# Kernel optimization log

Hardware: AMD Instinct MI355X
Metric: run time of the kernel (lower is better)

## Reference

```python
import jax, jax.numpy as jnp
import numpy as np

N_NODES = 100000
N_EDGES = 640000
IN_DIM = 128
HIDDEN = 256
OUT_DIM = 64


def setup_inputs() -> dict:
    key = jax.random.key(0)
    k_x, k_e, k_w1, k_b1, k_w2, k_b2 = jax.random.split(key, 6)
    x = jax.random.normal(k_x, (N_NODES, IN_DIM), dtype=jnp.float32)
    edge_index = jax.random.randint(k_e, (2, N_EDGES), 0, N_NODES, dtype=jnp.int32)
    # torch Linear init ~ U(-1/sqrt(fan_in), 1/sqrt(fan_in)); scale here is arbitrary for a correctness baseline
    s1 = 1.0 / np.sqrt(2 * IN_DIM)
    s2 = 1.0 / np.sqrt(HIDDEN)
    W1 = jax.random.uniform(k_w1, (2 * IN_DIM, HIDDEN), minval=-s1, maxval=s1, dtype=jnp.float32)
    b1 = jax.random.uniform(k_b1, (HIDDEN,), minval=-s1, maxval=s1, dtype=jnp.float32)
    W2 = jax.random.uniform(k_w2, (HIDDEN, OUT_DIM), minval=-s2, maxval=s2, dtype=jnp.float32)
    b2 = jax.random.uniform(k_b2, (OUT_DIM,), minval=-s2, maxval=s2, dtype=jnp.float32)
    return {"x": x, "edge_index": edge_index, "W1": W1, "b1": b1, "W2": W2, "b2": b2}


def reference(x, edge_index, W1, b1, W2, b2):
    # gather source/destination node features: [E, in_dim] each
    src = x[edge_index[0]]
    dst = x[edge_index[1]]
    h = jnp.concatenate([src, dst], axis=-1)      # [E, 2*in_dim]
    h = jax.nn.relu(h @ W1 + b1)                  # [E, hidden]
    return h @ W2 + b2                            # [E, out_dim]
```

## Files before the change

### kernel.cpp

```cpp
#include <hip/hip_runtime.h>
#include <hip/hip_bf16.h>


#define N_EDGES_C 640000
#define N_NODES_C 100000
#define IN_DIM_C  128
#define CAT_DIM_C 256
#define HIDDEN_C  256
#define OUT_DIM_C 64
#define BM        64
#define LDA       264

typedef __attribute__((ext_vector_type(8))) short bf16x8;
typedef __attribute__((ext_vector_type(4))) float f32x4;

__device__ __forceinline__ ushort f2bs(float f) {
  union { __hip_bfloat16 h; ushort u; } c;
  c.h = __float2bfloat16(f);
  return c.u;
}

__global__ __launch_bounds__(256) void cast_x_kernel(const float* __restrict__ x,
                                                     ushort* __restrict__ xb) {
  const int i = blockIdx.x * 256 + threadIdx.x;
  const float4 v0 = reinterpret_cast<const float4*>(x)[2 * i];
  const float4 v1 = reinterpret_cast<const float4*>(x)[2 * i + 1];
  uint4 o;
  o.x = (unsigned)f2bs(v0.x) | ((unsigned)f2bs(v0.y) << 16);
  o.y = (unsigned)f2bs(v0.z) | ((unsigned)f2bs(v0.w) << 16);
  o.z = (unsigned)f2bs(v1.x) | ((unsigned)f2bs(v1.y) << 16);
  o.w = (unsigned)f2bs(v1.z) | ((unsigned)f2bs(v1.w) << 16);
  reinterpret_cast<uint4*>(xb)[i] = o;
}

__global__ __launch_bounds__(256) void prep_w_kernel(const float* __restrict__ W1,
                                                     const float* __restrict__ W2,
                                                     ushort* __restrict__ W1t,
                                                     ushort* __restrict__ W2t) {
  const int i = blockIdx.x * 256 + threadIdx.x;
  if (i < HIDDEN_C * CAT_DIM_C) {
    const int n = i >> 8, k = i & 255;
    W1t[i] = f2bs(W1[k * HIDDEN_C + n]);
  } else {
    const int j = i - HIDDEN_C * CAT_DIM_C;
    const int o = j >> 8, k = j & 255;
    W2t[j] = f2bs(W2[k * OUT_DIM_C + o]);
  }
}

template <int USE_XB>
__global__ __launch_bounds__(256) void edge_ffn_kernel(
    const ushort* __restrict__ xb, const float* __restrict__ xf,
    const int* __restrict__ ei,
    const ushort* __restrict__ W1t, const float* __restrict__ b1,
    const ushort* __restrict__ W2t, const float* __restrict__ b2,
    float* __restrict__ out) {
  __shared__ ushort A[BM * LDA];

  const int tid  = threadIdx.x;
  const int lane = tid & 63;
  const int w    = tid >> 6;
  const int e0   = blockIdx.x * BM;
  const int l15  = lane & 15;
  const int lg   = lane >> 4;

  {
    const int li  = tid & 15;
    const int hr0 = tid >> 4;
#pragma unroll
    for (int it = 0; it < 8; ++it) {
      const int hr    = hr0 + it * 16;
      const int edge  = hr >> 1;
      const int which = hr & 1;
      const int node  = ei[which * N_EDGES_C + e0 + edge];
      ushort* dst = &A[edge * LDA + which * IN_DIM_C + li * 8];
      if (USE_XB) {
        *reinterpret_cast<uint4*>(dst) =
            *reinterpret_cast<const uint4*>(xb + node * IN_DIM_C + li * 8);
      } else {
        const float4* row = reinterpret_cast<const float4*>(xf + node * IN_DIM_C);
        const float4 v0 = row[li * 2];
        const float4 v1 = row[li * 2 + 1];
        uint4 o;
        o.x = (unsigned)f2bs(v0.x) | ((unsigned)f2bs(v0.y) << 16);
        o.y = (unsigned)f2bs(v0.z) | ((unsigned)f2bs(v0.w) << 16);
        o.z = (unsigned)f2bs(v1.x) | ((unsigned)f2bs(v1.y) << 16);
        o.w = (unsigned)f2bs(v1.z) | ((unsigned)f2bs(v1.w) << 16);
        *reinterpret_cast<uint4*>(dst) = o;
      }
    }
  }
  __syncthreads();

  f32x4 acc[4][4];
#pragma unroll
  for (int m = 0; m < 4; ++m)
#pragma unroll
    for (int n = 0; n < 4; ++n) acc[m][n] = (f32x4){0.f, 0.f, 0.f, 0.f};

#pragma unroll
  for (int ks = 0; ks < 8; ++ks) {
    const int kb = ks * 32 + lg * 8;
    bf16x8 a[4], b[4];
#pragma unroll
    for (int m = 0; m < 4; ++m)
      a[m] = *reinterpret_cast<const bf16x8*>(&A[(m * 16 + l15) * LDA + kb]);
#pragma unroll
    for (int n = 0; n < 4; ++n) {
      const int col = w * 64 + n * 16 + l15;
      b[n] = *reinterpret_cast<const bf16x8*>(W1t + col * CAT_DIM_C + kb);
    }
#pragma unroll
    for (int m = 0; m < 4; ++m)
#pragma unroll
      for (int n = 0; n < 4; ++n)
        acc[m][n] = __builtin_amdgcn_mfma_f32_16x16x32_bf16(a[m], b[n], acc[m][n], 0, 0, 0);
  }

  float b1v[4];
#pragma unroll
  for (int n = 0; n < 4; ++n) b1v[n] = b1[w * 64 + n * 16 + l15];

  __syncthreads();
#pragma unroll
  for (int m = 0; m < 4; ++m)
#pragma unroll
    for (int n = 0; n < 4; ++n)
#pragma unroll
      for (int i = 0; i < 4; ++i) {
        float v = acc[m][n][i] + b1v[n];
        v = v > 0.f ? v : 0.f;
        const int row = m * 16 + lg * 4 + i;
        const int col = w * 64 + n * 16 + l15;
        A[row * LDA + col] = f2bs(v);
      }
  __syncthreads();

  f32x4 acc2[4];
#pragma unroll
  for (int n = 0; n < 4; ++n) acc2[n] = (f32x4){0.f, 0.f, 0.f, 0.f};

#pragma unroll
  for (int ks = 0; ks < 8; ++ks) {
    const int kb = ks * 32 + lg * 8;
    const bf16x8 a2 = *reinterpret_cast<const bf16x8*>(&A[(w * 16 + l15) * LDA + kb]);
#pragma unroll
    for (int n = 0; n < 4; ++n) {
      const bf16x8 bb =
          *reinterpret_cast<const bf16x8*>(W2t + (n * 16 + l15) * HIDDEN_C + kb);
      acc2[n] = __builtin_amdgcn_mfma_f32_16x16x32_bf16(a2, bb, acc2[n], 0, 0, 0);
    }
  }

  float b2v[4];
#pragma unroll
  for (int n = 0; n < 4; ++n) b2v[n] = b2[n * 16 + l15];
#pragma unroll
  for (int n = 0; n < 4; ++n)
#pragma unroll
    for (int i = 0; i < 4; ++i) {
      const int row = e0 + w * 16 + lg * 4 + i;
      out[row * OUT_DIM_C + n * 16 + l15] = acc2[n][i] + b2v[n];
    }
}

extern "C" void kernel_launch(void* const* d_in, const int* in_sizes, int n_in,
                              void* d_out, int out_size, void* d_ws, size_t ws_size,
                              hipStream_t stream) {
  const float* x  = (const float*)d_in[0];
  const int*   ei = (const int*)d_in[1];
  const float* W1 = (const float*)d_in[2];
  const float* b1 = (const float*)d_in[3];
  const float* W2 = (const float*)d_in[4];
  const float* b2 = (const float*)d_in[5];
  float* out = (float*)d_out;

  const size_t xb_elems  = (size_t)N_NODES_C * IN_DIM_C;
  const size_t w1t_elems = HIDDEN_C * CAT_DIM_C;
  const size_t w2t_elems = OUT_DIM_C * HIDDEN_C;
  const size_t need_full = (xb_elems + w1t_elems + w2t_elems) * sizeof(ushort);

  ushort* base = (ushort*)d_ws;
  if (ws_size >= need_full) {
    ushort* xbp = base;
    ushort* W1t = xbp + xb_elems;
    ushort* W2t = W1t + w1t_elems;
    cast_x_kernel<<<(N_NODES_C * IN_DIM_C) / (256 * 8), 256, 0, stream>>>(x, xbp);
    prep_w_kernel<<<(HIDDEN_C * CAT_DIM_C + OUT_DIM_C * HIDDEN_C) / 256, 256, 0, stream>>>(
        W1, W2, W1t, W2t);
    edge_ffn_kernel<1><<<N_EDGES_C / BM, 256, 0, stream>>>(xbp, x, ei, W1t, b1, W2t, b2, out);
  } else {
    ushort* W1t = base;
    ushort* W2t = W1t + w1t_elems;
    prep_w_kernel<<<(HIDDEN_C * CAT_DIM_C + OUT_DIM_C * HIDDEN_C) / 256, 256, 0, stream>>>(
        W1, W2, W1t, W2t);
    edge_ffn_kernel<0><<<N_EDGES_C / BM, 256, 0, stream>>>(nullptr, x, ei, W1t, b1, W2t, b2, out);
  }
}
```

Baseline: 534.4 us.

## Make edge FFN kernel persistent over tiles with register-prefetched gathers

Each block now processes five 64-edge tiles instead of one, with the grid shrunk to cover that. The next tile's node-feature gather is issued into registers while the current tile's GEMMs run, and edge indices are loaded two tiles ahead, to hide gather latency. Bias loads are hoisted out of the tile loop and launch bounds request four blocks per CU. The cost is higher register pressure from the prefetch buffers and fewer, longer-running blocks.

New measurement: 1.129 ms. 2.11x slower.

```diff
diff --git a/kernel.cpp b/kernel.cpp
--- a/kernel.cpp
+++ b/kernel.cpp
@@ -10,6 +10,8 @@
 #define OUT_DIM_C 64
 #define BM        64
 #define LDA       264
+#define TPB_TILES 5
+#define GRID_MAIN 2000
 
 typedef __attribute__((ext_vector_type(8))) short bf16x8;
 typedef __attribute__((ext_vector_type(4))) float f32x4;
@@ -49,7 +51,7 @@
 }
 
 template <int USE_XB>
-__global__ __launch_bounds__(256) void edge_ffn_kernel(
+__global__ __launch_bounds__(256, 4) void edge_ffn_kernel(
     const ushort* __restrict__ xb, const float* __restrict__ xf,
     const int* __restrict__ ei,
     const ushort* __restrict__ W1t, const float* __restrict__ b1,
@@ -60,108 +62,133 @@
   const int tid  = threadIdx.x;
   const int lane = tid & 63;
   const int w    = tid >> 6;
-  const int e0   = blockIdx.x * BM;
   const int l15  = lane & 15;
   const int lg   = lane >> 4;
-
-  {
-    const int li  = tid & 15;
-    const int hr0 = tid >> 4;
+  const int li   = tid & 15;
+  const int hr0  = tid >> 4;
+  const int tile0 = blockIdx.x * TPB_TILES;
+
+  float b1v[4], b2v[4];
+#pragma unroll
+  for (int n = 0; n < 4; ++n) {
+    b1v[n] = b1[w * 64 + n * 16 + l15];
+    b2v[n] = b2[n * 16 + l15];
+  }
+
+  int   nid[8];
+  uint4 rbuf[8];
+
+#define LOAD_NID(tt)                                                        \
+  {                                                                         \
+    const int e0n = (tt) * BM;                                              \
+    _Pragma("unroll") for (int it = 0; it < 8; ++it) {                      \
+      const int hr = hr0 + it * 16;                                         \
+      nid[it] = ei[(hr & 1) * N_EDGES_C + e0n + (hr >> 1)];                 \
+    }                                                                       \
+  }
+
+#define GATHER()                                                            \
+  {                                                                         \
+    _Pragma("unroll") for (int it = 0; it < 8; ++it) {                      \
+      if (USE_XB) {                                                         \
+        rbuf[it] = *reinterpret_cast<const uint4*>(                         \
+            xb + (size_t)nid[it] * IN_DIM_C + li * 8);                      \
+      } else {                                                              \
+        const float4* row =                                                 \
+            reinterpret_cast<const float4*>(xf + (size_t)nid[it] * IN_DIM_C);\
+        const float4 v0 = row[li * 2];                                      \
+        const float4 v1 = row[li * 2 + 1];                                  \
+        uint4 o;                                                            \
+        o.x = (unsigned)f2bs(v0.x) | ((unsigned)f2bs(v0.y) << 16);          \
+        o.y = (unsigned)f2bs(v0.z) | ((unsigned)f2bs(v0.w) << 16);          \
+        o.z = (unsigned)f2bs(v1.x) | ((unsigned)f2bs(v1.y) << 16);          \
+        o.w = (unsigned)f2bs(v1.z) | ((unsigned)f2bs(v1.w) << 16);          \
+        rbuf[it] = o;                                                       \
+      }                                                                     \
+    }                                                                       \
+  }
+
+  LOAD_NID(tile0);
+  GATHER();
+  LOAD_NID(tile0 + 1);
+
+  for (int t = 0; t < TPB_TILES; ++t) {
+    const int e0 = (tile0 + t) * BM;
+
+    __syncthreads();
 #pragma unroll
     for (int it = 0; it < 8; ++it) {
-      const int hr    = hr0 + it * 16;
-      const int edge  = hr >> 1;
-      const int which = hr & 1;
-      const int node  = ei[which * N_EDGES_C + e0 + edge];
-      ushort* dst = &A[edge * LDA + which * IN_DIM_C + li * 8];
-      if (USE_XB) {
-        *reinterpret_cast<uint4*>(dst) =
-            *reinterpret_cast<const uint4*>(xb + node * IN_DIM_C + li * 8);
-      } else {
-        const float4* row = reinterpret_cast<const float4*>(xf + node * IN_DIM_C);
-        const float4 v0 = row[li * 2];
-        const float4 v1 = row[li * 2 + 1];
-        uint4 o;
-        o.x = (unsigned)f2bs(v0.x) | ((unsigned)f2bs(v0.y) << 16);
-        o.y = (unsigned)f2bs(v0.z) | ((unsigned)f2bs(v0.w) << 16);
-        o.z = (unsigned)f2bs(v1.x) | ((unsigned)f2bs(v1.y) << 16);
-        o.w = (unsigned)f2bs(v1.z) | ((unsigned)f2bs(v1.w) << 16);
-        *reinterpret_cast<uint4*>(dst) = o;
+      const int hr = hr0 + it * 16;
+      *reinterpret_cast<uint4*>(&A[(hr >> 1) * LDA + (hr & 1) * IN_DIM_C + li * 8]) =
+          rbuf[it];
+    }
+    __syncthreads();
+
+    f32x4 acc[4][4];
+#pragma unroll
+    for (int m = 0; m < 4; ++m)
+#pragma unroll
+      for (int n = 0; n < 4; ++n) acc[m][n] = (f32x4){0.f, 0.f, 0.f, 0.f};
+
+#pragma unroll
+    for (int ks = 0; ks < 8; ++ks) {
+      const int kb = ks * 32 + lg * 8;
+      bf16x8 a[4], b[4];
+#pragma unroll
+      for (int m = 0; m < 4; ++m)
+        a[m] = *reinterpret_cast<const bf16x8*>(&A[(m * 16 + l15) * LDA + kb]);
+#pragma unroll
+      for (int n = 0; n < 4; ++n)
+        b[n] = *reinterpret_cast<const bf16x8*>(W1t + (w * 64 + n * 16 + l15) * CAT_DIM_C + kb);
+#pragma unroll
+      for (int m = 0; m < 4; ++m)
+#pragma unroll
+        for (int n = 0; n < 4; ++n)
+          acc[m][n] = __builtin_amdgcn_mfma_f32_16x16x32_bf16(a[m], b[n], acc[m][n], 0, 0, 0);
+    }
+
+    if (t + 1 < TPB_TILES) GATHER();
+    if (t + 2 < TPB_TILES) LOAD_NID(tile0 + t + 2);
+
+    __syncthreads();
+
+#pragma unroll
+    for (int m = 0; m < 4; ++m)
+#pragma unroll
+      for (int n = 0; n < 4; ++n)
+#pragma unroll
+        for (int i = 0; i < 4; ++i) {
+          float v = acc[m][n][i] + b1v[n];
+          v = v > 0.f ? v : 0.f;
+          A[(m * 16 + lg * 4 + i) * LDA + w * 64 + n * 16 + l15] = f2bs(v);
+        }
+    __syncthreads();
+
+    f32x4 acc2[4];
+#pragma unroll
+    for (int n = 0; n < 4; ++n) acc2[n] = (f32x4){0.f, 0.f, 0.f, 0.f};
+
+#pragma unroll
+    for (int ks = 0; ks < 8; ++ks) {
+      const int kb = ks * 32 + lg * 8;
+      const bf16x8 a2 = *reinterpret_cast<const bf16x8*>(&A[(w * 16 + l15) * LDA + kb]);
+#pragma unroll
+      for (int n = 0; n < 4; ++n) {
+        const bf16x8 bb =
+            *reinterpret_cast<const bf16x8*>(W2t + (n * 16 + l15) * HIDDEN_C + kb);
+        acc2[n] = __builtin_amdgcn_mfma_f32_16x16x32_bf16(a2, bb, acc2[n], 0, 0, 0);
       }
     }
-  }
-  __syncthreads();
-
-  f32x4 acc[4][4];
-#pragma unroll
-  for (int m = 0; m < 4; ++m)
-#pragma unroll
-    for (int n = 0; n < 4; ++n) acc[m][n] = (f32x4){0.f, 0.f, 0.f, 0.f};
-
-#pragma unroll
-  for (int ks = 0; ks < 8; ++ks) {
-    const int kb = ks * 32 + lg * 8;
-    bf16x8 a[4], b[4];
-#pragma unroll
-    for (int m = 0; m < 4; ++m)
-      a[m] = *reinterpret_cast<const bf16x8*>(&A[(m * 16 + l15) * LDA + kb]);
-#pragma unroll
-    for (int n = 0; n < 4; ++n) {
-      const int col = w * 64 + n * 16 + l15;
-      b[n] = *reinterpret_cast<const bf16x8*>(W1t + col * CAT_DIM_C + kb);
-    }
-#pragma unroll
-    for (int m = 0; m < 4; ++m)
-#pragma unroll
-      for (int n = 0; n < 4; ++n)
-        acc[m][n] = __builtin_amdgcn_mfma_f32_16x16x32_bf16(a[m], b[n], acc[m][n], 0, 0, 0);
-  }
-
-  float b1v[4];
-#pragma unroll
-  for (int n = 0; n < 4; ++n) b1v[n] = b1[w * 64 + n * 16 + l15];
-
-  __syncthreads();
-#pragma unroll
-  for (int m = 0; m < 4; ++m)
+
 #pragma unroll
     for (int n = 0; n < 4; ++n)
 #pragma unroll
-      for (int i = 0; i < 4; ++i) {
-        float v = acc[m][n][i] + b1v[n];
-        v = v > 0.f ? v : 0.f;
-        const int row = m * 16 + lg * 4 + i;
-        const int col = w * 64 + n * 16 + l15;
-        A[row * LDA + col] = f2bs(v);
-      }
-  __syncthreads();
-
-  f32x4 acc2[4];
-#pragma unroll
-  for (int n = 0; n < 4; ++n) acc2[n] = (f32x4){0.f, 0.f, 0.f, 0.f};
-
-#pragma unroll
-  for (int ks = 0; ks < 8; ++ks) {
-    const int kb = ks * 32 + lg * 8;
-    const bf16x8 a2 = *reinterpret_cast<const bf16x8*>(&A[(w * 16 + l15) * LDA + kb]);
-#pragma unroll
-    for (int n = 0; n < 4; ++n) {
-      const bf16x8 bb =
-          *reinterpret_cast<const bf16x8*>(W2t + (n * 16 + l15) * HIDDEN_C + kb);
-      acc2[n] = __builtin_amdgcn_mfma_f32_16x16x32_bf16(a2, bb, acc2[n], 0, 0, 0);
-    }
-  }
-
-  float b2v[4];
-#pragma unroll
-  for (int n = 0; n < 4; ++n) b2v[n] = b2[n * 16 + l15];
-#pragma unroll
-  for (int n = 0; n < 4; ++n)
-#pragma unroll
-    for (int i = 0; i < 4; ++i) {
-      const int row = e0 + w * 16 + lg * 4 + i;
-      out[row * OUT_DIM_C + n * 16 + l15] = acc2[n][i] + b2v[n];
-    }
+      for (int i = 0; i < 4; ++i)
+        out[(size_t)(e0 + w * 16 + lg * 4 + i) * OUT_DIM_C + n * 16 + l15] =
+            acc2[n][i] + b2v[n];
+  }
+#undef LOAD_NID
+#undef GATHER
 }
 
 extern "C" void kernel_launch(void* const* d_in, const int* in_sizes, int n_in,
@@ -188,12 +215,12 @@
     cast_x_kernel<<<(N_NODES_C * IN_DIM_C) / (256 * 8), 256, 0, stream>>>(x, xbp);
     prep_w_kernel<<<(HIDDEN_C * CAT_DIM_C + OUT_DIM_C * HIDDEN_C) / 256, 256, 0, stream>>>(
         W1, W2, W1t, W2t);
-    edge_ffn_kernel<1><<<N_EDGES_C / BM, 256, 0, stream>>>(xbp, x, ei, W1t, b1, W2t, b2, out);
+    edge_ffn_kernel<1><<<GRID_MAIN, 256, 0, stream>>>(xbp, x, ei, W1t, b1, W2t, b2, out);
   } else {
     ushort* W1t = base;
     ushort* W2t = W1t + w1t_elems;
     prep_w_kernel<<<(HIDDEN_C * CAT_DIM_C + OUT_DIM_C * HIDDEN_C) / 256, 256, 0, stream>>>(
         W1, W2, W1t, W2t);
-    edge_ffn_kernel<0><<<N_EDGES_C / BM, 256, 0, stream>>>(nullptr, x, ei, W1t, b1, W2t, b2, out);
-  }
-}
+    edge_ffn_kernel<0><<<GRID_MAIN, 256, 0, stream>>>(nullptr, x, ei, W1t, b1, W2t, b2, out);
+  }
+}
```

## Fuse both GEMMs per wave with register-resident gathered features and chunked hidden

Applied to the files above, without the earlier changes.

Each wave now owns 32 edges. It gathers their source and destination features straight into registers as MFMA fragments, with no shared-memory staging tile. The hidden layer is computed in 32-column chunks: bias and ReLU are applied, the result goes through a small per-wave LDS buffer and is fed immediately into the second GEMM. This removes the block-wide syncs and the large shared tile, and raises edges per block to 128 with launch bounds asking for two blocks. In exchange, W1 and W2 fragments are reloaded per wave from global/L2, and register pressure rises from holding 16 feature fragments.

Result: slower. 627.8 us (+17.5%).

```diff
diff --git a/kernel.cpp b/kernel.cpp
--- a/kernel.cpp
+++ b/kernel.cpp
@@ -8,8 +8,8 @@
 #define CAT_DIM_C 256
 #define HIDDEN_C  256
 #define OUT_DIM_C 64
-#define BM        64
-#define LDA       264
+#define EPB       128
+#define GRID_MAIN (N_EDGES_C / EPB)
 
 typedef __attribute__((ext_vector_type(8))) short bf16x8;
 typedef __attribute__((ext_vector_type(4))) float f32x4;
@@ -49,119 +49,130 @@
 }
 
 template <int USE_XB>
-__global__ __launch_bounds__(256) void edge_ffn_kernel(
+__global__ __launch_bounds__(256, 2) void edge_ffn_kernel(
     const ushort* __restrict__ xb, const float* __restrict__ xf,
     const int* __restrict__ ei,
     const ushort* __restrict__ W1t, const float* __restrict__ b1,
     const ushort* __restrict__ W2t, const float* __restrict__ b2,
     float* __restrict__ out) {
-  __shared__ ushort A[BM * LDA];
-
-  const int tid  = threadIdx.x;
-  const int lane = tid & 63;
-  const int w    = tid >> 6;
-  const int e0   = blockIdx.x * BM;
-  const int l15  = lane & 15;
-  const int lg   = lane >> 4;
-
-  {
-    const int li  = tid & 15;
-    const int hr0 = tid >> 4;
-#pragma unroll
-    for (int it = 0; it < 8; ++it) {
-      const int hr    = hr0 + it * 16;
-      const int edge  = hr >> 1;
-      const int which = hr & 1;
-      const int node  = ei[which * N_EDGES_C + e0 + edge];
-      ushort* dst = &A[edge * LDA + which * IN_DIM_C + li * 8];
+  __shared__ ushort Hw[4][2][32][40];
+
+  const int tid = threadIdx.x;
+  const int l15 = tid & 15;
+  const int lg  = (tid >> 4) & 3;
+  const int wv  = tid >> 6;
+  const int e_base = blockIdx.x * EPB + wv * 32;
+
+  int ns[2], nd[2];
+#pragma unroll
+  for (int ef = 0; ef < 2; ++ef) {
+    const int e = e_base + ef * 16 + l15;
+    ns[ef] = ei[e];
+    nd[ef] = ei[N_EDGES_C + e];
+  }
+
+  bf16x8 xfr[2][8];
+#pragma unroll
+  for (int ef = 0; ef < 2; ++ef) {
+#pragma unroll
+    for (int ks = 0; ks < 8; ++ks) {
+      const int node = (ks < 4) ? ns[ef] : nd[ef];
+      const int koff = (ks & 3) * 32 + lg * 8;
       if (USE_XB) {
-        *reinterpret_cast<uint4*>(dst) =
-            *reinterpret_cast<const uint4*>(xb + node * IN_DIM_C + li * 8);
+        xfr[ef][ks] = *reinterpret_cast<const bf16x8*>(
+            xb + (size_t)node * IN_DIM_C + koff);
       } else {
-        const float4* row = reinterpret_cast<const float4*>(xf + node * IN_DIM_C);
-        const float4 v0 = row[li * 2];
-        const float4 v1 = row[li * 2 + 1];
+        const float4* row = reinterpret_cast<const float4*>(
+            xf + (size_t)node * IN_DIM_C + koff);
+        const float4 v0 = row[0];
+        const float4 v1 = row[1];
         uint4 o;
         o.x = (unsigned)f2bs(v0.x) | ((unsigned)f2bs(v0.y) << 16);
         o.y = (unsigned)f2bs(v0.z) | ((unsigned)f2bs(v0.w) << 16);
         o.z = (unsigned)f2bs(v1.x) | ((unsigned)f2bs(v1.y) << 16);
         o.w = (unsigned)f2bs(v1.z) | ((unsigned)f2bs(v1.w) << 16);
-        *reinterpret_cast<uint4*>(dst) = o;
+        xfr[ef][ks] = *reinterpret_cast<const bf16x8*>(&o);
       }
     }
   }
-  __syncthreads();
-
-  f32x4 acc[4][4];
-#pragma unroll
-  for (int m = 0; m < 4; ++m)
-#pragma unroll
-    for (int n = 0; n < 4; ++n) acc[m][n] = (f32x4){0.f, 0.f, 0.f, 0.f};
-
-#pragma unroll
-  for (int ks = 0; ks < 8; ++ks) {
-    const int kb = ks * 32 + lg * 8;
-    bf16x8 a[4], b[4];
-#pragma unroll
-    for (int m = 0; m < 4; ++m)
-      a[m] = *reinterpret_cast<const bf16x8*>(&A[(m * 16 + l15) * LDA + kb]);
-#pragma unroll
-    for (int n = 0; n < 4; ++n) {
-      const int col = w * 64 + n * 16 + l15;
-      b[n] = *reinterpret_cast<const bf16x8*>(W1t + col * CAT_DIM_C + kb);
-    }
-#pragma unroll
-    for (int m = 0; m < 4; ++m)
-#pragma unroll
-      for (int n = 0; n < 4; ++n)
-        acc[m][n] = __builtin_amdgcn_mfma_f32_16x16x32_bf16(a[m], b[n], acc[m][n], 0, 0, 0);
-  }
-
-  float b1v[4];
-#pragma unroll
-  for (int n = 0; n < 4; ++n) b1v[n] = b1[w * 64 + n * 16 + l15];
-
-  __syncthreads();
-#pragma unroll
-  for (int m = 0; m < 4; ++m)
-#pragma unroll
-    for (int n = 0; n < 4; ++n)
-#pragma unroll
-      for (int i = 0; i < 4; ++i) {
-        float v = acc[m][n][i] + b1v[n];
-        v = v > 0.f ? v : 0.f;
-        const int row = m * 16 + lg * 4 + i;
-        const int col = w * 64 + n * 16 + l15;
-        A[row * LDA + col] = f2bs(v);
+
+  f32x4 b2v[4];
+#pragma unroll
+  for (int of = 0; of < 4; ++of)
+    b2v[of] = *reinterpret_cast<const f32x4*>(b2 + of * 16 + lg * 4);
+
+  f32x4 acc2[4][2];
+#pragma unroll
+  for (int of = 0; of < 4; ++of)
+#pragma unroll
+    for (int ef = 0; ef < 2; ++ef) acc2[of][ef] = (f32x4){0.f, 0.f, 0.f, 0.f};
+
+#pragma unroll
+  for (int nb = 0; nb < 8; ++nb) {
+    f32x4 acc1[2][2];
+#pragma unroll
+    for (int np = 0; np < 2; ++np)
+#pragma unroll
+      for (int ef = 0; ef < 2; ++ef) acc1[np][ef] = (f32x4){0.f, 0.f, 0.f, 0.f};
+
+#pragma unroll
+    for (int np = 0; np < 2; ++np) {
+      const ushort* wrow = W1t + (size_t)(nb * 32 + np * 16 + l15) * CAT_DIM_C + lg * 8;
+#pragma unroll
+      for (int ks = 0; ks < 8; ++ks) {
+        const bf16x8 wf = *reinterpret_cast<const bf16x8*>(wrow + ks * 32);
+        acc1[np][0] = __builtin_amdgcn_mfma_f32_16x16x32_bf16(wf, xfr[0][ks], acc1[np][0], 0, 0, 0);
+        acc1[np][1] = __builtin_amdgcn_mfma_f32_16x16x32_bf16(wf, xfr[1][ks], acc1[np][1], 0, 0, 0);
       }
-  __syncthreads();
-
-  f32x4 acc2[4];
-#pragma unroll
-  for (int n = 0; n < 4; ++n) acc2[n] = (f32x4){0.f, 0.f, 0.f, 0.f};
-
-#pragma unroll
-  for (int ks = 0; ks < 8; ++ks) {
-    const int kb = ks * 32 + lg * 8;
-    const bf16x8 a2 = *reinterpret_cast<const bf16x8*>(&A[(w * 16 + l15) * LDA + kb]);
-#pragma unroll
-    for (int n = 0; n < 4; ++n) {
-      const bf16x8 bb =
-          *reinterpret_cast<const bf16x8*>(W2t + (n * 16 + l15) * HIDDEN_C + kb);
-      acc2[n] = __builtin_amdgcn_mfma_f32_16x16x32_bf16(a2, bb, acc2[n], 0, 0, 0);
-    }
-  }
-
-  float b2v[4];
-#pragma unroll
-  for (int n = 0; n < 4; ++n) b2v[n] = b2[n * 16 + l15];
-#pragma unroll
-  for (int n = 0; n < 4; ++n)
-#pragma unroll
-    for (int i = 0; i < 4; ++i) {
-      const int row = e0 + w * 16 + lg * 4 + i;
-      out[row * OUT_DIM_C + n * 16 + l15] = acc2[n][i] + b2v[n];
-    }
+    }
+
+#pragma unroll
+    for (int np = 0; np < 2; ++np) {
+      const f32x4 b1q = *reinterpret_cast<const f32x4*>(b1 + nb * 32 + np * 16 + lg * 4);
+#pragma unroll
+      for (int ef = 0; ef < 2; ++ef) {
+        float v0 = acc1[np][ef][0] + b1q[0];
+        float v1 = acc1[np][ef][1] + b1q[1];
+        float v2 = acc1[np][ef][2] + b1q[2];
+        float v3 = acc1[np][ef][3] + b1q[3];
+        v0 = v0 > 0.f ? v0 : 0.f;
+        v1 = v1 > 0.f ? v1 : 0.f;
+        v2 = v2 > 0.f ? v2 : 0.f;
+        v3 = v3 > 0.f ? v3 : 0.f;
+        uint2 u;
+        u.x = (unsigned)f2bs(v0) | ((unsigned)f2bs(v1) << 16);
+        u.y = (unsigned)f2bs(v2) | ((unsigned)f2bs(v3) << 16);
+        *reinterpret_cast<uint2*>(&Hw[wv][nb & 1][ef * 16 + l15][np * 16 + lg * 4]) = u;
+      }
+    }
+
+    bf16x8 hfrag[2];
+#pragma unroll
+    for (int ef = 0; ef < 2; ++ef)
+      hfrag[ef] = *reinterpret_cast<const bf16x8*>(&Hw[wv][nb & 1][ef * 16 + l15][lg * 8]);
+#pragma unroll
+    for (int of = 0; of < 4; ++of) {
+      const bf16x8 w2f = *reinterpret_cast<const bf16x8*>(
+          W2t + (size_t)(of * 16 + l15) * HIDDEN_C + nb * 32 + lg * 8);
+#pragma unroll
+      for (int ef = 0; ef < 2; ++ef)
+        acc2[of][ef] = __builtin_amdgcn_mfma_f32_16x16x32_bf16(w2f, hfrag[ef], acc2[of][ef], 0, 0, 0);
+    }
+  }
+
+#pragma unroll
+  for (int ef = 0; ef < 2; ++ef) {
+    const size_t erow = (size_t)(e_base + ef * 16 + l15) * OUT_DIM_C;
+#pragma unroll
+    for (int of = 0; of < 4; ++of) {
+      f32x4 v;
+      v[0] = acc2[of][ef][0] + b2v[of][0];
+      v[1] = acc2[of][ef][1] + b2v[of][1];
+      v[2] = acc2[of][ef][2] + b2v[of][2];
+      v[3] = acc2[of][ef][3] + b2v[of][3];
+      *reinterpret_cast<f32x4*>(out + erow + of * 16 + lg * 4) = v;
+    }
+  }
 }
 
 extern "C" void kernel_launch(void* const* d_in, const int* in_sizes, int n_in,
@@ -188,12 +199,12 @@
     cast_x_kernel<<<(N_NODES_C * IN_DIM_C) / (256 * 8), 256, 0, stream>>>(x, xbp);
     prep_w_kernel<<<(HIDDEN_C * CAT_DIM_C + OUT_DIM_C * HIDDEN_C) / 256, 256, 0, stream>>>(
         W1, W2, W1t, W2t);
-    edge_ffn_kernel<1><<<N_EDGES_C / BM, 256, 0, stream>>>(xbp, x, ei, W1t, b1, W2t, b2, out);
+    edge_ffn_kernel<1><<<GRID_MAIN, 256, 0, stream>>>(xbp, x, ei, W1t, b1, W2t, b2, out);
   } else {
     ushort* W1t = base;
     ushort* W2t = W1t + w1t_elems;
     prep_w_kernel<<<(HIDDEN_C * CAT_DIM_C + OUT_DIM_C * HIDDEN_C) / 256, 256, 0, stream>>>(
         W1, W2, W1t, W2t);
-    edge_ffn_kernel<0><<<N_EDGES_C / BM, 256, 0, stream>>>(nullptr, x, ei, W1t, b1, W2t, b2, out);
-  }
-}
+    edge_ffn_kernel<0><<<GRID_MAIN, 256, 0, stream>>>(nullptr, x, ei, W1t, b1, W2t, b2, out);
+  }
+}
```
